# Kernel optimization log

Measured on AMD Instinct MI355X. Metric: run time of the kernel, lower is better.

Reference implementation:

```python
import jax, jax.numpy as jnp
import numpy as np

HEAD_DIM = 64
NUM_HEADS = 32
ROPE_BASE = 10000.0


def _rope_interleaved(x):
    # x: [B, T, H, D]; interleaved RoPE on query, seqlen_offset = 0
    B, T, H, D = x.shape
    inv_freq = 1.0 / (ROPE_BASE ** (jnp.arange(0, D, 2, dtype=jnp.float32) / D))  # [D/2]
    t = jnp.arange(T, dtype=jnp.float32)
    freqs = t[:, None] * inv_freq[None, :]          # [T, D/2]
    cos = jnp.cos(freqs)[None, :, None, :]          # [1, T, 1, D/2]
    sin = jnp.sin(freqs)[None, :, None, :]
    x1 = x[..., 0::2]
    x2 = x[..., 1::2]
    o1 = x1 * cos - x2 * sin
    o2 = x1 * sin + x2 * cos
    out = jnp.stack([o1, o2], axis=-1).reshape(x.shape)  # re-interleave
    return out


def setup_inputs() -> dict:
    key = jax.random.key(0)
    k1, k2, k3, k4, k5 = jax.random.split(key, 5)
    B, T, Dm = 2, 2048, 2048
    H, Dh = NUM_HEADS, HEAD_DIM
    scale = 0.02
    return {
        "hidden_states": jax.random.normal(k1, (B, T, Dm), jnp.float32),
        "shared_k": jax.random.normal(k2, (B, T, H, Dh), jnp.float32),
        "shared_v": jax.random.normal(k3, (B, T, H, Dh), jnp.float32),
        "Wq": jax.random.normal(k4, (Dm, Dm), jnp.float32) * scale,
        "Wo": jax.random.normal(k5, (Dm, Dm), jnp.float32) * scale,
    }


def reference(hidden_states, shared_k, shared_v, Wq, Wo):
    B, T, Dm = hidden_states.shape
    H, Dh = NUM_HEADS, HEAD_DIM
    # q projection (nn.Linear: x @ W.T)
    q = (hidden_states @ Wq.T).reshape(B, T, H, Dh)
    # rotary on q only (seqlen_offset = shared_k_len - q_len = 0)
    q = _rope_interleaved(q)
    # parallel causal attention over shared KV cache (window_size=None)
    scale = 1.0 / jnp.sqrt(jnp.asarray(Dh, jnp.float32))
    scores = jnp.einsum('bqhd,bkhd->bhqk', q, shared_k) * scale
    causal = jnp.tril(jnp.ones((T, T), dtype=bool))
    scores = jnp.where(causal[None, None], scores, -jnp.inf)
    p = jax.nn.softmax(scores, axis=-1)
    o = jnp.einsum('bhqk,bkhd->bqhd', p, shared_v)
    o = o.reshape(B, T, Dm)
    return o @ Wo.T
```

## Files before the change

### kernel.cpp

```cpp
#include <hip/hip_runtime.h>
#include <stdint.h>

typedef short short8 __attribute__((ext_vector_type(8)));
typedef float f32x4 __attribute__((ext_vector_type(4)));

#define QSCALE 0.1803368801111137f
#define FREQC 0.4152410118609203f

__device__ __forceinline__ float bf2f(unsigned short u) {
    union { unsigned int i; float f; } x; x.i = ((unsigned int)u) << 16; return x.f;
}
__device__ __forceinline__ unsigned short f2bf(float f) {
    union { float f; unsigned int i; } x; x.f = f;
    unsigned int i = x.i;
    unsigned int r = i + 0x7FFFu + ((i >> 16) & 1u);
    return (unsigned short)(r >> 16);
}

#define GLDS16(g, l) \
    __builtin_amdgcn_global_load_lds((const __attribute__((address_space(1))) void*)(g), \
                                     (__attribute__((address_space(3))) void*)(l), 16, 0, 0)

__global__ void cvt_all(const float* __restrict__ hs, const float* __restrict__ k,
                        const float* __restrict__ wq, const float* __restrict__ wo,
                        unsigned short* __restrict__ hs_b, unsigned short* __restrict__ k_b,
                        unsigned short* __restrict__ wq_b, unsigned short* __restrict__ wo_b) {
    int blk = blockIdx.x;
    const float* in; unsigned short* out; int i;
    if (blk < 8192)        { in = hs; out = hs_b; i = blk * 256 + threadIdx.x; }
    else if (blk < 16384)  { in = k;  out = k_b;  i = (blk - 8192) * 256 + threadIdx.x; }
    else if (blk < 20480)  { in = wq; out = wq_b; i = (blk - 16384) * 256 + threadIdx.x; }
    else                   { in = wo; out = wo_b; i = (blk - 20480) * 256 + threadIdx.x; }
    float4 v = ((const float4*)in)[i];
    ushort4 o;
    o.x = f2bf(v.x); o.y = f2bf(v.y); o.z = f2bf(v.z); o.w = f2bf(v.w);
    ((ushort4*)out)[i] = o;
}

__global__ __launch_bounds__(256) void transpose_v(const float* __restrict__ V, unsigned short* __restrict__ Vt) {
    __shared__ float s[64 * 65];
    int t0 = blockIdx.x * 64;
    int bh = blockIdx.y;
    int b = bh >> 5, h = bh & 31;
    int tid = threadIdx.x;
#pragma unroll
    for (int it = 0; it < 4; ++it) {
        int c = tid + it * 256;
        int t = c >> 4;
        int d0 = (c & 15) * 4;
        float4 v = *(const float4*)(V + (size_t)(((b * 2048 + t0 + t) * 32 + h)) * 64 + d0);
        s[t * 65 + d0 + 0] = v.x; s[t * 65 + d0 + 1] = v.y;
        s[t * 65 + d0 + 2] = v.z; s[t * 65 + d0 + 3] = v.w;
    }
    __syncthreads();
#pragma unroll
    for (int it = 0; it < 2; ++it) {
        int c = tid + it * 256;
        int d = c >> 3;
        int tt = (c & 7) * 8;
        short8 pk;
#pragma unroll
        for (int j = 0; j < 8; ++j) pk[j] = (short)f2bf(s[(tt + j) * 65 + d]);
        *(short8*)(Vt + (size_t)(bh * 64 + d) * 2048 + t0 + tt) = pk;
    }
}

template <bool BF16_OUT>
__global__ __launch_bounds__(256) void gemm_bt(
    const unsigned short* __restrict__ A,
    const unsigned short* __restrict__ B,
    void* __restrict__ Cout,
    int M, int N, int K)
{
    __shared__ __align__(16) unsigned short lA[128 * 64];
    __shared__ __align__(16) unsigned short lB[128 * 64];
    int tid = threadIdx.x, lane = tid & 63, wave = tid >> 6;
    int wm = (wave >> 1) * 64, wn = (wave & 1) * 64;
    int m16 = lane & 15, q = lane >> 4;
    int rowBase = blockIdx.x * 128, colBase = blockIdx.y * 128;
    f32x4 acc[4][4] = {};

    int sr = lane >> 3;
    int g  = (lane & 7) ^ sr;
    const unsigned short* gAp = A + (size_t)(rowBase + wave * 32 + sr) * K + g * 8;
    const unsigned short* gBp = B + (size_t)(colBase + wave * 32 + sr) * K + g * 8;
    unsigned short* lAd = &lA[(wave * 32) * 64];
    unsigned short* lBd = &lB[(wave * 32) * 64];

    for (int k0 = 0; k0 < K; k0 += 64) {
        __syncthreads();
#pragma unroll
        for (int i = 0; i < 4; ++i) {
            GLDS16(gAp + (size_t)(8 * i) * K + k0, lAd + (8 * i) * 64);
            GLDS16(gBp + (size_t)(8 * i) * K + k0, lBd + (8 * i) * 64);
        }
        __syncthreads();
#pragma unroll
        for (int kk = 0; kk < 2; ++kk) {
            short8 af[4], bfr[4];
#pragma unroll
            for (int i = 0; i < 4; ++i) {
                int RA = wm + i * 16 + m16;
                af[i]  = *(const short8*)&lA[RA * 64 + (((kk * 4 + q) ^ (RA & 7)) * 8)];
                int RB = wn + i * 16 + m16;
                bfr[i] = *(const short8*)&lB[RB * 64 + (((kk * 4 + q) ^ (RB & 7)) * 8)];
            }
#pragma unroll
            for (int i = 0; i < 4; ++i)
#pragma unroll
                for (int jn = 0; jn < 4; ++jn)
                    acc[i][jn] = __builtin_amdgcn_mfma_f32_16x16x32_bf16(af[i], bfr[jn], acc[i][jn], 0, 0, 0);
        }
    }
#pragma unroll
    for (int i = 0; i < 4; ++i)
#pragma unroll
        for (int jn = 0; jn < 4; ++jn)
#pragma unroll
            for (int r = 0; r < 4; ++r) {
                int row = rowBase + wm + i * 16 + q * 4 + r;
                int col = colBase + wn + jn * 16 + m16;
                float v = acc[i][jn][r];
                if (BF16_OUT) ((unsigned short*)Cout)[(size_t)row * N + col] = f2bf(v);
                else          ((float*)Cout)[(size_t)row * N + col] = v;
            }
}

#define PROCESS(AQ0, AQ1, LRUN, ACCO, QT)                                          \
    do {                                                                           \
        bool diag = (kt == (QT));                                                  \
        _Pragma("unroll")                                                          \
        for (int nt = 0; nt < 4; ++nt) {                                           \
            f32x4 z = {0.f, 0.f, 0.f, 0.f};                                        \
            short8 bk0 = *(const short8*)&sK[(nt * 16 + m16) * SL + q * 8];        \
            short8 bk1 = *(const short8*)&sK[(nt * 16 + m16) * SL + 32 + q * 8];   \
            z = __builtin_amdgcn_mfma_f32_16x16x32_bf16(AQ0, bk0, z, 0, 0, 0);     \
            z = __builtin_amdgcn_mfma_f32_16x16x32_bf16(AQ1, bk1, z, 0, 0, 0);     \
            _Pragma("unroll")                                                      \
            for (int r = 0; r < 4; ++r) {                                          \
                float s = z[r];                                                    \
                if (diag) {                                                        \
                    int key = nt * 16 + m16;                                       \
                    int qi = w * 16 + q * 4 + r;                                   \
                    if (key > qi) s = -__builtin_inff();                           \
                }                                                                  \
                float pv = __builtin_amdgcn_exp2f(s);                              \
                LRUN[r] += pv;                                                     \
                sP[w][(q * 4 + r) * SL + nt * 16 + m16] = f2bf(pv);                \
            }                                                                      \
        }                                                                          \
        short8 ap0 = *(const short8*)&sP[w][m16 * SL + q * 8];                     \
        short8 ap1 = *(const short8*)&sP[w][m16 * SL + 32 + q * 8];                \
        _Pragma("unroll")                                                          \
        for (int nt = 0; nt < 4; ++nt) {                                           \
            short8 bv0 = *(const short8*)&sV[(nt * 16 + m16) * SL + q * 8];        \
            short8 bv1 = *(const short8*)&sV[(nt * 16 + m16) * SL + 32 + q * 8];   \
            ACCO[nt] = __builtin_amdgcn_mfma_f32_16x16x32_bf16(ap0, bv0, ACCO[nt], 0, 0, 0); \
            ACCO[nt] = __builtin_amdgcn_mfma_f32_16x16x32_bf16(ap1, bv1, ACCO[nt], 0, 0, 0); \
        }                                                                          \
    } while (0)

__global__ __launch_bounds__(256, 3) void attn(
    const unsigned short* __restrict__ Q,
    const unsigned short* __restrict__ Kb,
    const unsigned short* __restrict__ Vt,
    unsigned short* __restrict__ O)
{
    const int SL = 72;
    __shared__ __align__(16) unsigned short sK[64 * SL];
    __shared__ __align__(16) unsigned short sV[64 * SL];
    __shared__ __align__(16) unsigned short sP[4][16 * SL];
    int tid = threadIdx.x, lane = tid & 63, w = tid >> 6;
    int m16 = lane & 15, q = lane >> 4;
    int flat = blockIdx.x;
    int bh = flat & 63, p = flat >> 6;
    int b = bh >> 5, h = bh & 31;
    int qtA = 31 - p, qtB = p;

    short8 aqA0, aqA1, aqB0, aqB1;
    {
        int tA = qtA * 64 + w * 16 + m16;
        int tB = qtB * 64 + w * 16 + m16;
        const unsigned short* rowA = Q + (size_t)(b * 2048 + tA) * 2048 + h * 64 + q * 8;
        const unsigned short* rowB = Q + (size_t)(b * 2048 + tB) * 2048 + h * 64 + q * 8;
        short8 a0 = *(const short8*)rowA, a1 = *(const short8*)(rowA + 32);
        short8 b0 = *(const short8*)rowB, b1 = *(const short8*)(rowB + 32);
        float tfA = (float)tA, tfB = (float)tB;
#pragma unroll
        for (int j = 0; j < 4; ++j) {
            float inv0 = __builtin_amdgcn_exp2f(-FREQC * (float)(q * 4 + j));
            float inv1 = __builtin_amdgcn_exp2f(-FREQC * (float)(16 + q * 4 + j));
            float cA0 = __cosf(tfA * inv0), sA0 = __sinf(tfA * inv0);
            float cA1 = __cosf(tfA * inv1), sA1 = __sinf(tfA * inv1);
            float cB0 = __cosf(tfB * inv0), sB0 = __sinf(tfB * inv0);
            float cB1 = __cosf(tfB * inv1), sB1 = __sinf(tfB * inv1);
            float x1, x2;
            x1 = bf2f((unsigned short)a0[2 * j]); x2 = bf2f((unsigned short)a0[2 * j + 1]);
            aqA0[2 * j]     = (short)f2bf((x1 * cA0 - x2 * sA0) * QSCALE);
            aqA0[2 * j + 1] = (short)f2bf((x1 * sA0 + x2 * cA0) * QSCALE);
            x1 = bf2f((unsigned short)a1[2 * j]); x2 = bf2f((unsigned short)a1[2 * j + 1]);
            aqA1[2 * j]     = (short)f2bf((x1 * cA1 - x2 * sA1) * QSCALE);
            aqA1[2 * j + 1] = (short)f2bf((x1 * sA1 + x2 * cA1) * QSCALE);
            x1 = bf2f((unsigned short)b0[2 * j]); x2 = bf2f((unsigned short)b0[2 * j + 1]);
            aqB0[2 * j]     = (short)f2bf((x1 * cB0 - x2 * sB0) * QSCALE);
            aqB0[2 * j + 1] = (short)f2bf((x1 * sB0 + x2 * cB0) * QSCALE);
            x1 = bf2f((unsigned short)b1[2 * j]); x2 = bf2f((unsigned short)b1[2 * j + 1]);
            aqB1[2 * j]     = (short)f2bf((x1 * cB1 - x2 * sB1) * QSCALE);
            aqB1[2 * j + 1] = (short)f2bf((x1 * sB1 + x2 * cB1) * QSCALE);
        }
    }

    float lrunA[4] = {0.f, 0.f, 0.f, 0.f}, lrunB[4] = {0.f, 0.f, 0.f, 0.f};
    f32x4 accOA[4], accOB[4];
#pragma unroll
    for (int nt = 0; nt < 4; ++nt) {
        f32x4 z = {0.f, 0.f, 0.f, 0.f};
        accOA[nt] = z; accOB[nt] = z;
    }

    int cK = tid >> 3, c8 = tid & 7;
    const unsigned short* kbase = Kb + (size_t)(b * 2048) * 2048 + h * 64;
    const unsigned short* vbase = Vt + (size_t)((b * 32 + h) * 64) * 2048;

    for (int kt = 0; kt <= qtA; ++kt) {
        int kBase = kt * 64;
        __syncthreads();
#pragma unroll
        for (int it = 0; it < 2; ++it) {
            int row = cK + it * 32;
            *(float4*)&sK[row * SL + c8 * 8] =
                *(const float4*)(kbase + (size_t)(kBase + row) * 2048 + c8 * 8);
            *(float4*)&sV[row * SL + c8 * 8] =
                *(const float4*)(vbase + (size_t)row * 2048 + kBase + c8 * 8);
        }
        __syncthreads();

        PROCESS(aqA0, aqA1, lrunA, accOA, qtA);
        if (kt <= qtB) PROCESS(aqB0, aqB1, lrunB, accOB, qtB);
    }

#pragma unroll
    for (int r = 0; r < 4; ++r) {
        float la = lrunA[r], lb = lrunB[r];
        la += __shfl_xor(la, 1); lb += __shfl_xor(lb, 1);
        la += __shfl_xor(la, 2); lb += __shfl_xor(lb, 2);
        la += __shfl_xor(la, 4); lb += __shfl_xor(lb, 4);
        la += __shfl_xor(la, 8); lb += __shfl_xor(lb, 8);
        lrunA[r] = 1.0f / la; lrunB[r] = 1.0f / lb;
    }
#pragma unroll
    for (int nt = 0; nt < 4; ++nt)
#pragma unroll
        for (int r = 0; r < 4; ++r) {
            int col = h * 64 + nt * 16 + m16;
            O[(size_t)(b * 2048 + qtA * 64 + w * 16 + q * 4 + r) * 2048 + col] =
                f2bf(accOA[nt][r] * lrunA[r]);
            O[(size_t)(b * 2048 + qtB * 64 + w * 16 + q * 4 + r) * 2048 + col] =
                f2bf(accOB[nt][r] * lrunB[r]);
        }
}

extern "C" void kernel_launch(void* const* d_in, const int* in_sizes, int n_in,
                              void* d_out, int out_size, void* d_ws, size_t ws_size,
                              hipStream_t stream) {
    const float* hs = (const float*)d_in[0];
    const float* sk = (const float*)d_in[1];
    const float* sv = (const float*)d_in[2];
    const float* wq = (const float*)d_in[3];
    const float* wo = (const float*)d_in[4];
    float* out = (float*)d_out;

    char* ws = (char*)d_ws;
    unsigned short* hid_b = (unsigned short*)(ws);
    unsigned short* wq_b  = (unsigned short*)(ws + ((size_t)16 << 20));
    unsigned short* wo_b  = (unsigned short*)(ws + ((size_t)24 << 20));
    unsigned short* k_b   = (unsigned short*)(ws + ((size_t)32 << 20));
    unsigned short* vt_b  = (unsigned short*)(ws + ((size_t)48 << 20));
    unsigned short* q_b   = (unsigned short*)(ws + ((size_t)64 << 20));
    unsigned short* o_b   = (unsigned short*)(ws + ((size_t)80 << 20));

    cvt_all<<<24576, 256, 0, stream>>>(hs, sk, wq, wo, hid_b, k_b, wq_b, wo_b);
    transpose_v<<<dim3(32, 64), 256, 0, stream>>>(sv, vt_b);
    gemm_bt<true><<<dim3(32, 16), 256, 0, stream>>>(hid_b, wq_b, (void*)q_b, 4096, 2048, 2048);
    attn<<<1024, 256, 0, stream>>>(q_b, k_b, vt_b, o_b);
    gemm_bt<false><<<dim3(32, 16), 256, 0, stream>>>(o_b, wo_b, (void*)out, 4096, 2048, 2048);
}
```

Before: 329.5 us.

## Load attention K/V fragments directly to registers and halve GEMM N tile

The attention kernel no longer stages K and V tiles through shared memory with two barriers per key tile. Each wave now loads its MFMA B-operand fragments straight from global memory into registers, which removes the syncs and LDS traffic. Every wave fetches the same K/V data redundantly, so global/L2 traffic and register pressure go up. Separately, the GEMM tile shrinks from 128x128 to 128x64, doubling the grid to 1024 blocks for better CU occupancy at the cost of less data reuse per block.

```diff
diff --git a/kernel.cpp b/kernel.cpp
--- a/kernel.cpp
+++ b/kernel.cpp
@@ -73,49 +73,53 @@
     int M, int N, int K)
 {
     __shared__ __align__(16) unsigned short lA[128 * 64];
-    __shared__ __align__(16) unsigned short lB[128 * 64];
+    __shared__ __align__(16) unsigned short lB[64 * 64];
     int tid = threadIdx.x, lane = tid & 63, wave = tid >> 6;
-    int wm = (wave >> 1) * 64, wn = (wave & 1) * 64;
+    int wm = (wave >> 1) * 64, wn = (wave & 1) * 32;
     int m16 = lane & 15, q = lane >> 4;
-    int rowBase = blockIdx.x * 128, colBase = blockIdx.y * 128;
-    f32x4 acc[4][4] = {};
+    int rowBase = blockIdx.x * 128, colBase = blockIdx.y * 64;
+    f32x4 acc[4][2] = {};
 
     int sr = lane >> 3;
     int g  = (lane & 7) ^ sr;
     const unsigned short* gAp = A + (size_t)(rowBase + wave * 32 + sr) * K + g * 8;
-    const unsigned short* gBp = B + (size_t)(colBase + wave * 32 + sr) * K + g * 8;
+    const unsigned short* gBp = B + (size_t)(colBase + wave * 16 + sr) * K + g * 8;
     unsigned short* lAd = &lA[(wave * 32) * 64];
-    unsigned short* lBd = &lB[(wave * 32) * 64];
+    unsigned short* lBd = &lB[(wave * 16) * 64];
 
     for (int k0 = 0; k0 < K; k0 += 64) {
         __syncthreads();
 #pragma unroll
-        for (int i = 0; i < 4; ++i) {
+        for (int i = 0; i < 4; ++i)
             GLDS16(gAp + (size_t)(8 * i) * K + k0, lAd + (8 * i) * 64);
+#pragma unroll
+        for (int i = 0; i < 2; ++i)
             GLDS16(gBp + (size_t)(8 * i) * K + k0, lBd + (8 * i) * 64);
-        }
         __syncthreads();
 #pragma unroll
         for (int kk = 0; kk < 2; ++kk) {
-            short8 af[4], bfr[4];
+            short8 af[4], bfr[2];
 #pragma unroll
             for (int i = 0; i < 4; ++i) {
                 int RA = wm + i * 16 + m16;
                 af[i]  = *(const short8*)&lA[RA * 64 + (((kk * 4 + q) ^ (RA & 7)) * 8)];
-                int RB = wn + i * 16 + m16;
-                bfr[i] = *(const short8*)&lB[RB * 64 + (((kk * 4 + q) ^ (RB & 7)) * 8)];
             }
 #pragma unroll
+            for (int j = 0; j < 2; ++j) {
+                int RB = wn + j * 16 + m16;
+                bfr[j] = *(const short8*)&lB[RB * 64 + (((kk * 4 + q) ^ (RB & 7)) * 8)];
+            }
+#pragma unroll
             for (int i = 0; i < 4; ++i)
 #pragma unroll
-                for (int jn = 0; jn < 4; ++jn)
+                for (int jn = 0; jn < 2; ++jn)
                     acc[i][jn] = __builtin_amdgcn_mfma_f32_16x16x32_bf16(af[i], bfr[jn], acc[i][jn], 0, 0, 0);
         }
     }
 #pragma unroll
     for (int i = 0; i < 4; ++i)
 #pragma unroll
-        for (int jn = 0; jn < 4; ++jn)
+        for (int jn = 0; jn < 2; ++jn)
 #pragma unroll
             for (int r = 0; r < 4; ++r) {
                 int row = rowBase + wm + i * 16 + q * 4 + r;
@@ -132,10 +136,8 @@
         _Pragma("unroll")                                                          \
         for (int nt = 0; nt < 4; ++nt) {                                           \
             f32x4 z = {0.f, 0.f, 0.f, 0.f};                                        \
-            short8 bk0 = *(const short8*)&sK[(nt * 16 + m16) * SL + q * 8];        \
-            short8 bk1 = *(const short8*)&sK[(nt * 16 + m16) * SL + 32 + q * 8];   \
-            z = __builtin_amdgcn_mfma_f32_16x16x32_bf16(AQ0, bk0, z, 0, 0, 0);     \
-            z = __builtin_amdgcn_mfma_f32_16x16x32_bf16(AQ1, bk1, z, 0, 0, 0);     \
+            z = __builtin_amdgcn_mfma_f32_16x16x32_bf16(AQ0, kf[nt][0], z, 0, 0, 0); \
+            z = __builtin_amdgcn_mfma_f32_16x16x32_bf16(AQ1, kf[nt][1], z, 0, 0, 0); \
             _Pragma("unroll")                                                      \
             for (int r = 0; r < 4; ++r) {                                          \
                 float s = z[r];                                                    \
@@ -153,10 +155,8 @@
         short8 ap1 = *(const short8*)&sP[w][m16 * SL + 32 + q * 8];                \
         _Pragma("unroll")                                                          \
         for (int nt = 0; nt < 4; ++nt) {                                           \
-            short8 bv0 = *(const short8*)&sV[(nt * 16 + m16) * SL + q * 8];        \
-            short8 bv1 = *(const short8*)&sV[(nt * 16 + m16) * SL + 32 + q * 8];   \
-            ACCO[nt] = __builtin_amdgcn_mfma_f32_16x16x32_bf16(ap0, bv0, ACCO[nt], 0, 0, 0); \
-            ACCO[nt] = __builtin_amdgcn_mfma_f32_16x16x32_bf16(ap1, bv1, ACCO[nt], 0, 0, 0); \
+            ACCO[nt] = __builtin_amdgcn_mfma_f32_16x16x32_bf16(ap0, vf[nt][0], ACCO[nt], 0, 0, 0); \
+            ACCO[nt] = __builtin_amdgcn_mfma_f32_16x16x32_bf16(ap1, vf[nt][1], ACCO[nt], 0, 0, 0); \
         }                                                                          \
     } while (0)
 
@@ -166,9 +166,7 @@
     const unsigned short* __restrict__ Vt,
     unsigned short* __restrict__ O)
 {
-    const int SL = 72;
-    __shared__ __align__(16) unsigned short sK[64 * SL];
-    __shared__ __align__(16) unsigned short sV[64 * SL];
+    const int SL = 68;
     __shared__ __align__(16) unsigned short sP[4][16 * SL];
     int tid = threadIdx.x, lane = tid & 63, w = tid >> 6;
     int m16 = lane & 15, q = lane >> 4;
@@ -218,23 +216,20 @@
         accOA[nt] = z; accOB[nt] = z;
     }
 
-    int cK = tid >> 3, c8 = tid & 7;
-    const unsigned short* kbase = Kb + (size_t)(b * 2048) * 2048 + h * 64;
-    const unsigned short* vbase = Vt + (size_t)((b * 32 + h) * 64) * 2048;
+    const unsigned short* kptr = Kb + ((size_t)(b * 2048 + m16)) * 2048 + h * 64 + q * 8;
+    const unsigned short* vptr = Vt + ((size_t)((b * 32 + h) * 64 + m16)) * 2048 + q * 8;
 
     for (int kt = 0; kt <= qtA; ++kt) {
-        int kBase = kt * 64;
-        __syncthreads();
-#pragma unroll
-        for (int it = 0; it < 2; ++it) {
-            int row = cK + it * 32;
-            *(float4*)&sK[row * SL + c8 * 8] =
-                *(const float4*)(kbase + (size_t)(kBase + row) * 2048 + c8 * 8);
-            *(float4*)&sV[row * SL + c8 * 8] =
-                *(const float4*)(vbase + (size_t)row * 2048 + kBase + c8 * 8);
-        }
-        __syncthreads();
-
+        short8 kf[4][2], vf[4][2];
+#pragma unroll
+        for (int nt = 0; nt < 4; ++nt) {
+            const unsigned short* kp = kptr + (size_t)(kt * 64 + nt * 16) * 2048;
+            kf[nt][0] = *(const short8*)kp;
+            kf[nt][1] = *(const short8*)(kp + 32);
+            const unsigned short* vp = vptr + (size_t)(nt * 16) * 2048 + kt * 64;
+            vf[nt][0] = *(const short8*)vp;
+            vf[nt][1] = *(const short8*)(vp + 32);
+        }
         PROCESS(aqA0, aqA1, lrunA, accOA, qtA);
         if (kt <= qtB) PROCESS(aqB0, aqB1, lrunB, accOB, qtB);
     }
@@ -281,7 +276,7 @@
 
     cvt_all<<<24576, 256, 0, stream>>>(hs, sk, wq, wo, hid_b, k_b, wq_b, wo_b);
     transpose_v<<<dim3(32, 64), 256, 0, stream>>>(sv, vt_b);
-    gemm_bt<true><<<dim3(32, 16), 256, 0, stream>>>(hid_b, wq_b, (void*)q_b, 4096, 2048, 2048);
+    gemm_bt<true><<<dim3(32, 32), 256, 0, stream>>>(hid_b, wq_b, (void*)q_b, 4096, 2048, 2048);
     attn<<<1024, 256, 0, stream>>>(q_b, k_b, vt_b, o_b);
-    gemm_bt<false><<<dim3(32, 16), 256, 0, stream>>>(o_b, wo_b, (void*)out, 4096, 2048, 2048);
-}
+    gemm_bt<false><<<dim3(32, 32), 256, 0, stream>>>(o_b, wo_b, (void*)out, 4096, 2048, 2048);
+}
```

Measured after the change: 484.4 us. 1.47x slower.
